# Performance work log

Measured on AMD Instinct MI355X. Metric: run time of the kernel, lower is better.

Reference implementation:

```python
import jax, jax.numpy as jnp
import numpy as np

EMB = 1024
HEADS = 16


def setup_inputs() -> dict:
    key = jax.random.key(0)
    ks = jax.random.split(key, 9)
    s = 1.0 / np.sqrt(EMB)
    x = jax.random.normal(ks[0], (2, 2048, EMB), dtype=jnp.float32)
    Wq = jax.random.normal(ks[1], (EMB, EMB), dtype=jnp.float32) * s
    bq = jnp.zeros((EMB,), dtype=jnp.float32)
    Wk = jax.random.normal(ks[2], (EMB, EMB), dtype=jnp.float32) * s
    bk = jnp.zeros((EMB,), dtype=jnp.float32)
    Wv = jax.random.normal(ks[3], (EMB, EMB), dtype=jnp.float32) * s
    bv = jnp.zeros((EMB,), dtype=jnp.float32)
    Wo = jax.random.normal(ks[4], (EMB, EMB), dtype=jnp.float32) * s
    bo = jnp.zeros((EMB,), dtype=jnp.float32)
    return {"x": x, "Wq": Wq, "bq": bq, "Wk": Wk, "bk": bk,
            "Wv": Wv, "bv": bv, "Wo": Wo, "bo": bo}


def reference(x, Wq, bq, Wk, bk, Wv, bv, Wo, bo):
    b, n, e = x.shape
    h = HEADS
    d = e // h
    # q/k/v projections -> [b, h, n, d]
    def split_heads(t):
        return t.reshape(b, n, h, d).transpose(0, 2, 1, 3)
    q = split_heads(x @ Wq.T + bq)
    k = split_heads(x @ Wk.T + bk)
    v = split_heads(x @ Wv.T + bv)
    # NOTE: original scales by sqrt(emb_size), not sqrt(head_dim)
    scaling = jnp.sqrt(jnp.float32(e))
    energy = jnp.einsum('bhqd,bhkd->bhqk', q, k)  # [b,h,n,n]
    att = jax.nn.softmax(energy / scaling, axis=-1)
    out = jnp.einsum('bhqk,bhkd->bhqd', att, v)
    out = out.transpose(0, 2, 1, 3).reshape(b, n, e)
    return out @ Wo.T + bo
```

## Files before the change

### kernel.cpp

```cpp
#include <hip/hip_runtime.h>


typedef short short8  __attribute__((ext_vector_type(8)));
typedef float floatx4 __attribute__((ext_vector_type(4)));

#define SEQ   2048
#define BATCH 2
#define NH    16
#define HD    64
#define EMB   1024

#define QSCALE 0.045084220027780106f

__device__ __forceinline__ unsigned short f32_bf16(float f) {
    unsigned int u = __float_as_uint(f);
    u += 0x7FFF + ((u >> 16) & 1);
    return (unsigned short)(u >> 16);
}

__device__ __forceinline__ unsigned int pk_bf16(float lo, float hi) {
    return __builtin_amdgcn_perm(__float_as_uint(hi) + 0x8000u,
                                 __float_as_uint(lo) + 0x8000u, 0x07060302u);
}

__device__ __forceinline__ void gl_lds16(const unsigned short* g,
                                         unsigned short* l) {
    __builtin_amdgcn_global_load_lds(
        (const __attribute__((address_space(1))) unsigned int*)g,
        (__attribute__((address_space(3))) unsigned int*)l, 16, 0, 0);
}

__global__ __launch_bounds__(256) void convert_all(
        const float* __restrict__ x,  const float* __restrict__ wq,
        const float* __restrict__ wk, const float* __restrict__ wv,
        const float* __restrict__ wo, unsigned short* __restrict__ dst) {
    int i = (blockIdx.x * 256 + threadIdx.x) * 4;
    const float* src; int off;
    if      (i < 4194304) { src = x;  off = 0; }
    else if (i < 5242880) { src = wq; off = 4194304; }
    else if (i < 6291456) { src = wk; off = 5242880; }
    else if (i < 7340032) { src = wv; off = 6291456; }
    else                  { src = wo; off = 7340032; }
    float4 v = *(const float4*)(src + (i - off));
    uint2 o;
    o.x = pk_bf16(v.x, v.y);
    o.y = pk_bf16(v.z, v.w);
    *(uint2*)(dst + i) = o;
}

template <int MODE>
__device__ __forceinline__ void gemm_bt_core(
        unsigned short (* __restrict__ sA)[64],
        unsigned short (* __restrict__ sB)[64],
        const unsigned short* __restrict__ A,
        const unsigned short* __restrict__ B,
        const float* __restrict__ bias,
        unsigned short* __restrict__ outb) {
    const int t    = threadIdx.x;
    const int wave = t >> 6, lane = t & 63;
    const int l15  = lane & 15, quad = lane >> 4;
    const int wm   = (wave >> 1) * 64, wn = (wave & 1) * 64;
    const int m0   = blockIdx.y * 128,  n0 = blockIdx.x * 128;
    const int srow = lane >> 3;
    const int sch  = ((lane & 7) ^ srow) * 8;

    floatx4 acc[4][4] = {};

    for (int k0 = 0; k0 < EMB; k0 += 64) {
        for (int i = 0; i < 4; ++i) {
            int rr  = wave * 32 + i * 8;
            int row = rr + srow;
            gl_lds16(&A[(size_t)(m0 + row) * EMB + k0 + sch], &sA[0][0] + rr * 64);
            gl_lds16(&B[(size_t)(n0 + row) * EMB + k0 + sch], &sB[0][0] + rr * 64);
        }
        __syncthreads();
        for (int ks = 0; ks < 2; ++ks) {
            const int ch = (((ks * 4) + quad) ^ (l15 & 7)) * 8;
            short8 af[4], bf[4];
            for (int i = 0; i < 4; ++i)
                af[i] = *(const short8*)&sA[wm + i * 16 + l15][ch];
            for (int j = 0; j < 4; ++j)
                bf[j] = *(const short8*)&sB[wn + j * 16 + l15][ch];
            for (int i = 0; i < 4; ++i)
                for (int j = 0; j < 4; ++j)
                    acc[i][j] = __builtin_amdgcn_mfma_f32_16x16x32_bf16(
                        af[i], bf[j], acc[i][j], 0, 0, 0);
        }
        __syncthreads();
    }
    if (MODE == 2) {
        for (int i = 0; i < 4; ++i) {
            int row = m0 + wm + i * 16 + quad * 4;
            int bb  = row >> 11, seq = row & 2047;
            for (int j = 0; j < 4; ++j) {
                int col = n0 + wn + j * 16 + l15;
                float bv = bias[col];
                int vtrow = (bb * 16 + (col >> 6)) * 64 + (col & 63);
                uint2 pk;
                pk.x = pk_bf16(acc[i][j][0] + bv, acc[i][j][1] + bv);
                pk.y = pk_bf16(acc[i][j][2] + bv, acc[i][j][3] + bv);
                *(uint2*)&outb[(size_t)vtrow * SEQ + seq] = pk;
            }
        }
    } else {
        const float sc2 = (MODE == 1) ? QSCALE : 1.0f;
        for (int i = 0; i < 4; ++i) {
            int row = m0 + wm + i * 16 + quad * 4;
            for (int j = 0; j < 4; ++j) {
                int col = n0 + wn + j * 16 + l15;
                float bv = bias[col];
                for (int r = 0; r < 4; ++r) {
                    float v = (acc[i][j][r] + bv) * sc2;
                    outb[(size_t)(row + r) * EMB + col] = f32_bf16(v);
                }
            }
        }
    }
}

__global__ __launch_bounds__(256, 3) void gemm_qkv(
        const unsigned short* __restrict__ xb,
        const unsigned short* __restrict__ wq,
        const unsigned short* __restrict__ wk,
        const unsigned short* __restrict__ wv,
        const float* __restrict__ bq, const float* __restrict__ bk,
        const float* __restrict__ bv,
        unsigned short* __restrict__ Q, unsigned short* __restrict__ K,
        unsigned short* __restrict__ VT) {
    __shared__ unsigned short sA[128][64];
    __shared__ unsigned short sB[128][64];
    if      (blockIdx.z == 0) gemm_bt_core<1>(sA, sB, xb, wq, bq, Q);
    else if (blockIdx.z == 1) gemm_bt_core<0>(sA, sB, xb, wk, bk, K);
    else                      gemm_bt_core<2>(sA, sB, xb, wv, bv, VT);
}

__global__ __launch_bounds__(256) void gemm_out(
        const unsigned short* __restrict__ A,
        const unsigned short* __restrict__ B,
        const float* __restrict__ bias, float* __restrict__ out) {
    __shared__ unsigned short sA[128][64];
    __shared__ unsigned short sB[64][64];
    const int t    = threadIdx.x;
    const int wave = t >> 6, lane = t & 63;
    const int l15  = lane & 15, quad = lane >> 4;
    const int wm   = wave * 32;
    const int m0   = blockIdx.y * 128,  n0 = blockIdx.x * 64;
    const int srow = lane >> 3;
    const int sch  = ((lane & 7) ^ srow) * 8;

    floatx4 acc[2][4] = {};

    for (int k0 = 0; k0 < EMB; k0 += 64) {
        {
            for (int i = 0; i < 4; ++i) {
                int rr = wave * 32 + i * 8;
                gl_lds16(&A[(size_t)(m0 + rr + srow) * EMB + k0 + sch],
                         &sA[0][0] + rr * 64);
            }
            for (int i = 0; i < 2; ++i) {
                int rr = wave * 16 + i * 8;
                gl_lds16(&B[(size_t)(n0 + rr + srow) * EMB + k0 + sch],
                         &sB[0][0] + rr * 64);
            }
        }
        __syncthreads();
        for (int ks = 0; ks < 2; ++ks) {
            const int ch = (((ks * 4) + quad) ^ (l15 & 7)) * 8;
            short8 af[2], bf[4];
            for (int i = 0; i < 2; ++i)
                af[i] = *(const short8*)&sA[wm + i * 16 + l15][ch];
            for (int j = 0; j < 4; ++j)
                bf[j] = *(const short8*)&sB[j * 16 + l15][ch];
            for (int i = 0; i < 2; ++i)
                for (int j = 0; j < 4; ++j)
                    acc[i][j] = __builtin_amdgcn_mfma_f32_16x16x32_bf16(
                        af[i], bf[j], acc[i][j], 0, 0, 0);
        }
        __syncthreads();
    }
    for (int i = 0; i < 2; ++i) {
        int row = m0 + wm + i * 16 + quad * 4;
        for (int j = 0; j < 4; ++j) {
            int col = n0 + j * 16 + l15;
            float bv = bias[col];
            for (int r = 0; r < 4; ++r)
                out[(size_t)(row + r) * EMB + col] = acc[i][j][r] + bv;
        }
    }
}

__global__ __launch_bounds__(256) void attn(
        const unsigned short* __restrict__ Q,
        const unsigned short* __restrict__ K,
        const unsigned short* __restrict__ VT,
        unsigned short* __restrict__ O) {
    __shared__ unsigned short sK [3][64][64];
    __shared__ unsigned short sVT[3][64][64];
    __shared__ unsigned short sP [128][72];
    const int t    = threadIdx.x;
    const int wave = t >> 6, lane = t & 63;
    const int l15  = lane & 15, quad = lane >> 4;
    const int bh   = blockIdx.x;
    const int b    = bh >> 4, h = bh & 15;
    const int q0   = blockIdx.y * 128;
    const size_t rowbase = (size_t)b * SEQ;
    const int colbase  = h * HD;
    const size_t vtbase = (size_t)bh * HD * SEQ;
    const int srow = lane >> 3;
    const int sch  = ((lane & 7) ^ srow) * 8;

    short8 qf[2][2];
    for (int g = 0; g < 2; ++g)
        for (int ks = 0; ks < 2; ++ks)
            qf[g][ks] = *(const short8*)
                &Q[(rowbase + q0 + wave * 32 + g * 16 + l15) * EMB
                   + colbase + ks * 32 + quad * 8];

    float l_part[2] = {0.f, 0.f};
    floatx4 o_acc[2][4] = {};

    for (int i = 0; i < 2; ++i) {
        int rr  = wave * 16 + i * 8;
        int row = rr + srow;
        gl_lds16(&K[(rowbase + row) * EMB + colbase + sch],
                 &sK[0][0][0] + rr * 64);
        gl_lds16(&VT[vtbase + (size_t)row * SEQ + sch],
                 &sVT[0][0][0] + rr * 64);
    }

    int cur = 0;
    for (int it = 0; it < SEQ / 64; ++it) {
        if (it < SEQ / 64 - 1) {
            int nb = cur + 1; if (nb == 3) nb = 0;
            int kt = (it + 1) * 64;
            for (int i = 0; i < 2; ++i) {
                int rr  = wave * 16 + i * 8;
                int row = rr + srow;
                gl_lds16(&K[(rowbase + kt + row) * EMB + colbase + sch],
                         &sK[nb][0][0] + rr * 64);
                gl_lds16(&VT[vtbase + (size_t)row * SEQ + kt + sch],
                         &sVT[nb][0][0] + rr * 64);
            }
            asm volatile("s_waitcnt vmcnt(4)" ::: "memory");
        } else {
            asm volatile("s_waitcnt vmcnt(0)" ::: "memory");
        }
        asm volatile("s_barrier" ::: "memory");

        const unsigned short (*cK)[64]  = sK[cur];
        const unsigned short (*cVT)[64] = sVT[cur];

        floatx4 s[2][4] = {};
        for (int ks = 0; ks < 2; ++ks) {
            const int ch = (((ks * 4) + quad) ^ (l15 & 7)) * 8;
            short8 kf[4];
            for (int mi = 0; mi < 4; ++mi)
                kf[mi] = *(const short8*)&cK[mi * 16 + l15][ch];
            for (int g = 0; g < 2; ++g)
                for (int mi = 0; mi < 4; ++mi)
                    s[g][mi] = __builtin_amdgcn_mfma_f32_16x16x32_bf16(
                        kf[mi], qf[g][ks], s[g][mi], 0, 0, 0);
        }

        for (int g = 0; g < 2; ++g) {
            int prow = wave * 32 + g * 16 + l15;
            float lp = l_part[g];
            for (int mi = 0; mi < 4; ++mi) {
                float p0 = __builtin_amdgcn_exp2f(s[g][mi][0]);
                float p1 = __builtin_amdgcn_exp2f(s[g][mi][1]);
                float p2 = __builtin_amdgcn_exp2f(s[g][mi][2]);
                float p3 = __builtin_amdgcn_exp2f(s[g][mi][3]);
                lp += (p0 + p1) + (p2 + p3);
                uint2 pk;
                pk.x = pk_bf16(p0, p1);
                pk.y = pk_bf16(p2, p3);
                *(uint2*)&sP[prow][mi * 16 + quad * 4] = pk;
            }
            l_part[g] = lp;
        }

        for (int ks = 0; ks < 2; ++ks) {
            const int ch = (((ks * 4) + quad) ^ (l15 & 7)) * 8;
            short8 vf[4];
            for (int mi = 0; mi < 4; ++mi)
                vf[mi] = *(const short8*)&cVT[mi * 16 + l15][ch];
            for (int g = 0; g < 2; ++g) {
                short8 pf = *(const short8*)
                    &sP[wave * 32 + g * 16 + l15][ks * 32 + quad * 8];
                for (int mi = 0; mi < 4; ++mi)
                    o_acc[g][mi] = __builtin_amdgcn_mfma_f32_16x16x32_bf16(
                        vf[mi], pf, o_acc[g][mi], 0, 0, 0);
            }
        }
        cur = cur + 1; if (cur == 3) cur = 0;
    }

    for (int g = 0; g < 2; ++g) {
        float la = l_part[g];
        la += __shfl_xor(la, 16, 64);
        la += __shfl_xor(la, 32, 64);
        const float inv_l = 1.0f / la;
        int prow = wave * 32 + g * 16 + l15;
        for (int mi = 0; mi < 4; ++mi) {
            uint2 pk;
            pk.x = pk_bf16(o_acc[g][mi][0] * inv_l, o_acc[g][mi][1] * inv_l);
            pk.y = pk_bf16(o_acc[g][mi][2] * inv_l, o_acc[g][mi][3] * inv_l);
            *(uint2*)&sP[prow][mi * 16 + quad * 4] = pk;
        }
    }
    __builtin_amdgcn_s_waitcnt(0);
    const int ql = lane >> 2, dh = (lane & 3) * 16;
    for (int g = 0; g < 2; ++g) {
        const size_t grow = rowbase + q0 + wave * 32 + g * 16 + ql;
        for (int i = 0; i < 2; ++i) {
            uint4 v = *(const uint4*)&sP[wave * 32 + g * 16 + ql][dh + i * 8];
            *(uint4*)&O[grow * EMB + colbase + dh + i * 8] = v;
        }
    }
}

extern "C" void kernel_launch(void* const* d_in, const int* in_sizes, int n_in,
                              void* d_out, int out_size, void* d_ws, size_t ws_size,
                              hipStream_t stream) {
    const float* x  = (const float*)d_in[0];
    const float* Wq = (const float*)d_in[1];
    const float* bq = (const float*)d_in[2];
    const float* Wk = (const float*)d_in[3];
    const float* bk = (const float*)d_in[4];
    const float* Wv = (const float*)d_in[5];
    const float* bv = (const float*)d_in[6];
    const float* Wo = (const float*)d_in[7];
    const float* bo = (const float*)d_in[8];

    unsigned short* ws  = (unsigned short*)d_ws;
    unsigned short* xb  = ws;
    unsigned short* wqb = ws + 4194304;
    unsigned short* wkb = ws + 5242880;
    unsigned short* wvb = ws + 6291456;
    unsigned short* wob = ws + 7340032;
    unsigned short* Qb  = ws + 8388608;
    unsigned short* Kb  = ws + 12582912;
    unsigned short* VTb = ws + 16777216;
    unsigned short* Ob  = ws + 20971520;

    convert_all<<<8192, 256, 0, stream>>>(x, Wq, Wk, Wv, Wo, ws);
    gemm_qkv<<<dim3(8, 32, 3), 256, 0, stream>>>(xb, wqb, wkb, wvb,
                                                 bq, bk, bv, Qb, Kb, VTb);
    attn<<<dim3(32, 16), 256, 0, stream>>>(Qb, Kb, VTb, Ob);
    gemm_out<<<dim3(16, 32), 256, 0, stream>>>(Ob, wob, bo, (float*)d_out);
}
```

Measured before the change: 191.0 us.

## Split attention KV tile across wave pairs with 512-thread blocks and reduce partials

Result: faster. 179.9 us (-5.8%).

```diff
diff --git a/kernel.cpp b/kernel.cpp
--- a/kernel.cpp
+++ b/kernel.cpp
@@ -189,16 +189,19 @@
     }
 }
 
-__global__ __launch_bounds__(256) void attn(
+__global__ __launch_bounds__(512) void attn(
         const unsigned short* __restrict__ Q,
         const unsigned short* __restrict__ K,
         const unsigned short* __restrict__ VT,
         unsigned short* __restrict__ O) {
-    __shared__ unsigned short sK [3][64][64];
-    __shared__ unsigned short sVT[3][64][64];
-    __shared__ unsigned short sP [128][72];
+    __shared__ __align__(16) unsigned short smem[33792];
+    unsigned short (*sK )[64][64] = (unsigned short (*)[64][64])(smem);
+    unsigned short (*sVT)[64][64] = (unsigned short (*)[64][64])(smem + 12288);
+    unsigned short (*sP )[72]     = (unsigned short (*)[72])(smem + 24576);
+
     const int t    = threadIdx.x;
     const int wave = t >> 6, lane = t & 63;
+    const int qh   = wave >> 1, kh = wave & 1;
     const int l15  = lane & 15, quad = lane >> 4;
     const int bh   = blockIdx.x;
     const int b    = bh >> 4, h = bh & 15;
@@ -213,35 +216,28 @@
     for (int g = 0; g < 2; ++g)
         for (int ks = 0; ks < 2; ++ks)
             qf[g][ks] = *(const short8*)
-                &Q[(rowbase + q0 + wave * 32 + g * 16 + l15) * EMB
+                &Q[(rowbase + q0 + qh * 32 + g * 16 + l15) * EMB
                    + colbase + ks * 32 + quad * 8];
 
     float l_part[2] = {0.f, 0.f};
     floatx4 o_acc[2][4] = {};
 
-    for (int i = 0; i < 2; ++i) {
-        int rr  = wave * 16 + i * 8;
-        int row = rr + srow;
-        gl_lds16(&K[(rowbase + row) * EMB + colbase + sch],
-                 &sK[0][0][0] + rr * 64);
-        gl_lds16(&VT[vtbase + (size_t)row * SEQ + sch],
-                 &sVT[0][0][0] + rr * 64);
-    }
+    const int rr  = wave * 8;
+    const int row = rr + srow;
+
+    gl_lds16(&K[(rowbase + row) * EMB + colbase + sch], &sK[0][0][0] + rr * 64);
+    gl_lds16(&VT[vtbase + (size_t)row * SEQ + sch],     &sVT[0][0][0] + rr * 64);
 
     int cur = 0;
     for (int it = 0; it < SEQ / 64; ++it) {
         if (it < SEQ / 64 - 1) {
             int nb = cur + 1; if (nb == 3) nb = 0;
             int kt = (it + 1) * 64;
-            for (int i = 0; i < 2; ++i) {
-                int rr  = wave * 16 + i * 8;
-                int row = rr + srow;
-                gl_lds16(&K[(rowbase + kt + row) * EMB + colbase + sch],
-                         &sK[nb][0][0] + rr * 64);
-                gl_lds16(&VT[vtbase + (size_t)row * SEQ + kt + sch],
-                         &sVT[nb][0][0] + rr * 64);
-            }
-            asm volatile("s_waitcnt vmcnt(4)" ::: "memory");
+            gl_lds16(&K[(rowbase + kt + row) * EMB + colbase + sch],
+                     &sK[nb][0][0] + rr * 64);
+            gl_lds16(&VT[vtbase + (size_t)row * SEQ + kt + sch],
+                     &sVT[nb][0][0] + rr * 64);
+            asm volatile("s_waitcnt vmcnt(2)" ::: "memory");
         } else {
             asm volatile("s_waitcnt vmcnt(0)" ::: "memory");
         }
@@ -250,43 +246,43 @@
         const unsigned short (*cK)[64]  = sK[cur];
         const unsigned short (*cVT)[64] = sVT[cur];
 
-        floatx4 s[2][4] = {};
+        floatx4 s[2][2] = {};
         for (int ks = 0; ks < 2; ++ks) {
             const int ch = (((ks * 4) + quad) ^ (l15 & 7)) * 8;
-            short8 kf[4];
-            for (int mi = 0; mi < 4; ++mi)
-                kf[mi] = *(const short8*)&cK[mi * 16 + l15][ch];
+            short8 kf[2];
+            for (int m = 0; m < 2; ++m)
+                kf[m] = *(const short8*)&cK[kh * 32 + m * 16 + l15][ch];
             for (int g = 0; g < 2; ++g)
-                for (int mi = 0; mi < 4; ++mi)
-                    s[g][mi] = __builtin_amdgcn_mfma_f32_16x16x32_bf16(
-                        kf[mi], qf[g][ks], s[g][mi], 0, 0, 0);
+                for (int m = 0; m < 2; ++m)
+                    s[g][m] = __builtin_amdgcn_mfma_f32_16x16x32_bf16(
+                        kf[m], qf[g][ks], s[g][m], 0, 0, 0);
         }
 
         for (int g = 0; g < 2; ++g) {
-            int prow = wave * 32 + g * 16 + l15;
+            int prow = qh * 32 + g * 16 + l15;
             float lp = l_part[g];
-            for (int mi = 0; mi < 4; ++mi) {
-                float p0 = __builtin_amdgcn_exp2f(s[g][mi][0]);
-                float p1 = __builtin_amdgcn_exp2f(s[g][mi][1]);
-                float p2 = __builtin_amdgcn_exp2f(s[g][mi][2]);
-                float p3 = __builtin_amdgcn_exp2f(s[g][mi][3]);
+            for (int m = 0; m < 2; ++m) {
+                float p0 = __builtin_amdgcn_exp2f(s[g][m][0]);
+                float p1 = __builtin_amdgcn_exp2f(s[g][m][1]);
+                float p2 = __builtin_amdgcn_exp2f(s[g][m][2]);
+                float p3 = __builtin_amdgcn_exp2f(s[g][m][3]);
                 lp += (p0 + p1) + (p2 + p3);
                 uint2 pk;
                 pk.x = pk_bf16(p0, p1);
                 pk.y = pk_bf16(p2, p3);
-                *(uint2*)&sP[prow][mi * 16 + quad * 4] = pk;
+                *(uint2*)&sP[prow][kh * 32 + m * 16 + quad * 4] = pk;
             }
             l_part[g] = lp;
         }
 
-        for (int ks = 0; ks < 2; ++ks) {
-            const int ch = (((ks * 4) + quad) ^ (l15 & 7)) * 8;
+        {
+            const int ch = ((kh * 4 + quad) ^ (l15 & 7)) * 8;
             short8 vf[4];
             for (int mi = 0; mi < 4; ++mi)
                 vf[mi] = *(const short8*)&cVT[mi * 16 + l15][ch];
             for (int g = 0; g < 2; ++g) {
                 short8 pf = *(const short8*)
-                    &sP[wave * 32 + g * 16 + l15][ks * 32 + quad * 8];
+                    &sP[qh * 32 + g * 16 + l15][kh * 32 + quad * 8];
                 for (int mi = 0; mi < 4; ++mi)
                     o_acc[g][mi] = __builtin_amdgcn_mfma_f32_16x16x32_bf16(
                         vf[mi], pf, o_acc[g][mi], 0, 0, 0);
@@ -295,26 +291,50 @@
         cur = cur + 1; if (cur == 3) cur = 0;
     }
 
+    float la[2];
     for (int g = 0; g < 2; ++g) {
-        float la = l_part[g];
-        la += __shfl_xor(la, 16, 64);
-        la += __shfl_xor(la, 32, 64);
-        const float inv_l = 1.0f / la;
-        int prow = wave * 32 + g * 16 + l15;
-        for (int mi = 0; mi < 4; ++mi) {
-            uint2 pk;
-            pk.x = pk_bf16(o_acc[g][mi][0] * inv_l, o_acc[g][mi][1] * inv_l);
-            pk.y = pk_bf16(o_acc[g][mi][2] * inv_l, o_acc[g][mi][3] * inv_l);
-            *(uint2*)&sP[prow][mi * 16 + quad * 4] = pk;
-        }
-    }
-    __builtin_amdgcn_s_waitcnt(0);
-    const int ql = lane >> 2, dh = (lane & 3) * 16;
-    for (int g = 0; g < 2; ++g) {
-        const size_t grow = rowbase + q0 + wave * 32 + g * 16 + ql;
-        for (int i = 0; i < 2; ++i) {
-            uint4 v = *(const uint4*)&sP[wave * 32 + g * 16 + ql][dh + i * 8];
-            *(uint4*)&O[grow * EMB + colbase + dh + i * 8] = v;
+        float v = l_part[g];
+        v += __shfl_xor(v, 16, 64);
+        v += __shfl_xor(v, 32, 64);
+        la[g] = v;
+    }
+
+    __syncthreads();
+    float* oscr = (float*)smem;
+    float* lscr = (float*)smem + 128 * 68;
+    if (kh == 1) {
+        for (int g = 0; g < 2; ++g) {
+            int q = qh * 32 + g * 16 + l15;
+            for (int mi = 0; mi < 4; ++mi)
+                *(floatx4*)&oscr[q * 68 + mi * 16 + quad * 4] = o_acc[g][mi];
+            if (quad == 0) lscr[q] = la[g];
+        }
+    }
+    __syncthreads();
+    if (kh == 0) {
+        for (int g = 0; g < 2; ++g) {
+            int q = qh * 32 + g * 16 + l15;
+            const float inv_l = 1.0f / (la[g] + lscr[q]);
+            for (int mi = 0; mi < 4; ++mi) {
+                floatx4 o1 = *(const floatx4*)&oscr[q * 68 + mi * 16 + quad * 4];
+                float c0 = (o_acc[g][mi][0] + o1[0]) * inv_l;
+                float c1 = (o_acc[g][mi][1] + o1[1]) * inv_l;
+                float c2 = (o_acc[g][mi][2] + o1[2]) * inv_l;
+                float c3 = (o_acc[g][mi][3] + o1[3]) * inv_l;
+                uint2 pk;
+                pk.x = pk_bf16(c0, c1);
+                pk.y = pk_bf16(c2, c3);
+                *(uint2*)&sP[q][mi * 16 + quad * 4] = pk;
+            }
+        }
+        __builtin_amdgcn_s_waitcnt(0);
+        const int ql = lane >> 2, dh = (lane & 3) * 16;
+        for (int g = 0; g < 2; ++g) {
+            const size_t grow = rowbase + q0 + qh * 32 + g * 16 + ql;
+            for (int i = 0; i < 2; ++i) {
+                uint4 v = *(const uint4*)&sP[qh * 32 + g * 16 + ql][dh + i * 8];
+                *(uint4*)&O[grow * EMB + colbase + dh + i * 8] = v;
+            }
         }
     }
 }
@@ -346,6 +366,6 @@
     convert_all<<<8192, 256, 0, stream>>>(x, Wq, Wk, Wv, Wo, ws);
     gemm_qkv<<<dim3(8, 32, 3), 256, 0, stream>>>(xb, wqb, wkb, wvb,
                                                  bq, bk, bv, Qb, Kb, VTb);
-    attn<<<dim3(32, 16), 256, 0, stream>>>(Qb, Kb, VTb, Ob);
+    attn<<<dim3(32, 16), 512, 0, stream>>>(Qb, Kb, VTb, Ob);
     gemm_out<<<dim3(16, 32), 256, 0, stream>>>(Ob, wob, bo, (float*)d_out);
 }
```
